# Performance work log

Hardware: AMD Instinct MI355X
Metric: run time of the kernel (lower is better)

The kernel has to match this reference:

```python
import jax, jax.numpy as jnp
import numpy as np

N, E, F, HID, HEADS, G = 20000, 320000, 64, 64, 4, 64
HC = HEADS * HID  # 256
NHID, NOUT = 256, 128
INV_SQRT2 = 0.7071067811865476


def _gat(x, src, dst, W, a_s, a_d, bias):
    # GATConv (v1), eval mode (no dropout); src/dst already include self-loops (PyG default)
    H, C = a_s.shape
    h = (x @ W).reshape(-1, H, C)  # [N,H,C]
    al_s = jnp.einsum('nhc,hc->nh', h, a_s)
    al_d = jnp.einsum('nhc,hc->nh', h, a_d)
    e = jax.nn.leaky_relu(al_s[src] + al_d[dst], 0.2)  # [Etot,H]
    m = jax.ops.segment_max(e, dst, num_segments=N)
    ex = jnp.exp(e - m[dst])
    den = jax.ops.segment_sum(ex, dst, num_segments=N)
    coef = ex / den[dst]  # softmax over incoming edges per target node
    out = jax.ops.segment_sum(h[src] * coef[:, :, None], dst, num_segments=N)
    return out.reshape(-1, H * C) + bias


def _bn(h, g, b):
    # BatchNorm1d, training-mode stats (biased var), eps=1e-5
    mu = h.mean(axis=0)
    var = h.var(axis=0)
    return g * (h - mu) * jax.lax.rsqrt(var + 1e-5) + b


def _block(x, src, dst, W1, a1s, a1d, b1, g1, be1, W2, a2s, a2d, b2, g2, be2, Wr, br, Wf, bf):
    h = jax.nn.relu(_bn(_gat(x, src, dst, W1, a1s, a1d, b1), g1, be1))
    h = jax.nn.relu(_bn(_gat(h, src, dst, W2, a2s, a2d, b2), g2, be2))
    res = x @ Wr + br
    return ((h + res) * INV_SQRT2) @ Wf + bf


def setup_inputs():
    ks = iter(jax.random.split(jax.random.key(0), 64))
    def rn(shape, scale=0.05):
        return jax.random.normal(next(ks), shape, dtype=jnp.float32) * scale
    inp = {}
    inp['x'] = jax.random.normal(next(ks), (N, F), dtype=jnp.float32)
    inp['edge_index'] = jax.random.randint(next(ks), (2, E), 0, N, dtype=jnp.int32)
    inp['batch'] = jnp.sort(jax.random.randint(next(ks), (N,), 0, G, dtype=jnp.int32))
    for b, cin in enumerate([F, HID]):
        p = 'b%d_' % b
        inp[p + 'W1'] = rn((cin, HC)); inp[p + 'a1s'] = rn((HEADS, HID)); inp[p + 'a1d'] = rn((HEADS, HID))
        inp[p + 'b1'] = jnp.zeros((HC,), jnp.float32)
        inp[p + 'g1'] = jnp.ones((HC,), jnp.float32); inp[p + 'be1'] = jnp.zeros((HC,), jnp.float32)
        inp[p + 'W2'] = rn((HC, HC)); inp[p + 'a2s'] = rn((1, HC)); inp[p + 'a2d'] = rn((1, HC))
        inp[p + 'b2'] = jnp.zeros((HC,), jnp.float32)
        inp[p + 'g2'] = jnp.ones((HC,), jnp.float32); inp[p + 'be2'] = jnp.zeros((HC,), jnp.float32)
        inp[p + 'Wr'] = rn((cin, HC)); inp[p + 'br'] = jnp.zeros((HC,), jnp.float32)
        inp[p + 'Wf'] = rn((HC, HID)); inp[p + 'bf'] = jnp.zeros((HID,), jnp.float32)
    inp['Wh1'] = rn((HID, NHID)); inp['bh1'] = jnp.zeros((NHID,), jnp.float32)
    inp['Wh2'] = rn((NHID, NOUT)); inp['bh2'] = jnp.zeros((NOUT,), jnp.float32)
    return inp


def reference(x, edge_index, batch,
              b0_W1, b0_a1s, b0_a1d, b0_b1, b0_g1, b0_be1, b0_W2, b0_a2s, b0_a2d, b0_b2, b0_g2, b0_be2, b0_Wr, b0_br, b0_Wf, b0_bf,
              b1_W1, b1_a1s, b1_a1d, b1_b1, b1_g1, b1_be1, b1_W2, b1_a2s, b1_a2d, b1_b2, b1_g2, b1_be2, b1_Wr, b1_br, b1_Wf, b1_bf,
              Wh1, bh1, Wh2, bh2):
    loops = jnp.arange(N, dtype=edge_index.dtype)
    src = jnp.concatenate([edge_index[0], loops])
    dst = jnp.concatenate([edge_index[1], loops])
    x = _block(x, src, dst, b0_W1, b0_a1s, b0_a1d, b0_b1, b0_g1, b0_be1, b0_W2, b0_a2s, b0_a2d, b0_b2, b0_g2, b0_be2, b0_Wr, b0_br, b0_Wf, b0_bf)
    x = _block(x, src, dst, b1_W1, b1_a1s, b1_a1d, b1_b1, b1_g1, b1_be1, b1_W2, b1_a2s, b1_a2d, b1_b2, b1_g2, b1_be2, b1_Wr, b1_br, b1_Wf, b1_bf)
    cnt = jax.ops.segment_sum(jnp.ones((N,), x.dtype), batch, num_segments=G)
    pooled = jax.ops.segment_sum(x, batch, num_segments=G) / jnp.maximum(cnt, 1.0)[:, None]
    h = jax.nn.relu(pooled @ Wh1 + bh1)
    return h @ Wh2 + bh2
```

## Files before the change

kernel.cpp:

```cpp
#include <hip/hip_runtime.h>

#define N_NODES 20000
#define N_EDGES 320000
#define ETOT (N_EDGES + N_NODES)
#define G_GROUPS 64

__device__ __forceinline__ unsigned short f2bf(float f) {
    unsigned int u = __float_as_uint(f);
    u += 0x7fffu + ((u >> 16) & 1u);
    return (unsigned short)(u >> 16);
}
__device__ __forceinline__ float bf2f(unsigned short v) {
    return __uint_as_float(((unsigned int)v) << 16);
}


__global__ __launch_bounds__(256) void k_hist(const int* __restrict__ ei, int* __restrict__ counts) {
    int e = blockIdx.x * 256 + threadIdx.x;
    if (e >= ETOT) return;
    int dst = (e < N_EDGES) ? ei[N_EDGES + e] : (e - N_EDGES);
    atomicAdd(&counts[dst], 1);
}

__global__ __launch_bounds__(1024) void k_scan(const int* __restrict__ counts, int* __restrict__ offs,
                                               int* __restrict__ cursor) {
    __shared__ int sdata[1024];
    const int t = threadIdx.x;
    const int chunk = (N_NODES + 1023) / 1024;
    int base = t * chunk;
    int s = 0;
    for (int i = 0; i < chunk; i++) { int idx = base + i; if (idx < N_NODES) s += counts[idx]; }
    sdata[t] = s;
    __syncthreads();
    for (int off = 1; off < 1024; off <<= 1) {
        int v = (t >= off) ? sdata[t - off] : 0;
        __syncthreads();
        sdata[t] += v;
        __syncthreads();
    }
    int prefix = (t == 0) ? 0 : sdata[t - 1];
    for (int i = 0; i < chunk; i++) {
        int idx = base + i;
        if (idx < N_NODES) {
            int cv = counts[idx];
            offs[idx] = prefix;
            cursor[idx] = prefix;
            prefix += cv;
        }
    }
    if (t == 1023) offs[N_NODES] = sdata[1023];
}

__global__ __launch_bounds__(256) void k_scatter(const int* __restrict__ ei, int* __restrict__ cursor,
                                                 int* __restrict__ csr_src) {
    int e = blockIdx.x * 256 + threadIdx.x;
    if (e >= ETOT) return;
    int src = (e < N_EDGES) ? ei[e] : (e - N_EDGES);
    int dst = (e < N_EDGES) ? ei[N_EDGES + e] : (e - N_EDGES);
    int p = atomicAdd(&cursor[dst], 1);
    csr_src[p] = src;
}


__global__ __launch_bounds__(256) void k_gemm64_dual(const float* __restrict__ x, const float* __restrict__ W1,
                                                     const float* __restrict__ Wr, const float* __restrict__ br,
                                                     const float* __restrict__ a_s, const float* __restrict__ a_d,
                                                     unsigned short* __restrict__ hbf, float* __restrict__ res,
                                                     float* __restrict__ alS, float* __restrict__ alD) {
    const int rb = blockIdx.x >> 2, cs = blockIdx.x & 3;
    const int row0 = rb * 64;
    const int nrows = min(64, N_NODES - row0);
    const int t = threadIdx.x;
    __shared__ float xs[32 * 68];
    __shared__ float b1s[32 * 64];
    __shared__ float brs[32 * 64];
    const int lane = t & 63;
    const int c0 = (t & 15) * 4;
    const int r0 = (t >> 4) * 4;
    const int rl = (t & 15) | ((t >> 6) << 4);
    const int c4 = (t >> 4) & 3;
    float acc1[4][4] = {}, acc2[4][4] = {};
    for (int k0 = 0; k0 < 64; k0 += 32) {
        if (k0) __syncthreads();
        {
            #pragma unroll
            for (int jj = 0; jj < 2; jj++) {
                int cc = c4 + 4 * jj;
                float4 v = {0.f, 0.f, 0.f, 0.f};
                if (rl < nrows) v = *(const float4*)(x + (row0 + rl) * 64 + k0 + cc * 4);
                xs[(cc * 4 + 0) * 68 + rl] = v.x;
                xs[(cc * 4 + 1) * 68 + rl] = v.y;
                xs[(cc * 4 + 2) * 68 + rl] = v.z;
                xs[(cc * 4 + 3) * 68 + rl] = v.w;
            }
        }
        {
            int cc = (t & 15) * 4;
            int k = t >> 4;
            #pragma unroll
            for (int pass = 0; pass < 2; pass++, k += 16) {
                *(float4*)(b1s + k * 64 + cc) = *(const float4*)(W1 + (k0 + k) * 256 + cs * 64 + cc);
                *(float4*)(brs + k * 64 + cc) = *(const float4*)(Wr + (k0 + k) * 256 + cs * 64 + cc);
            }
        }
        __syncthreads();
        #pragma unroll 8
        for (int k = 0; k < 32; k++) {
            float4 av = *(const float4*)(xs + k * 68 + r0);
            float4 b1 = *(const float4*)(b1s + k * 64 + c0);
            float4 b2 = *(const float4*)(brs + k * 64 + c0);
            float a[4] = {av.x, av.y, av.z, av.w};
            #pragma unroll
            for (int i = 0; i < 4; i++) {
                acc1[i][0] += a[i] * b1.x; acc1[i][1] += a[i] * b1.y;
                acc1[i][2] += a[i] * b1.z; acc1[i][3] += a[i] * b1.w;
                acc2[i][0] += a[i] * b2.x; acc2[i][1] += a[i] * b2.y;
                acc2[i][2] += a[i] * b2.z; acc2[i][3] += a[i] * b2.w;
            }
        }
    }
    const int gcol = cs * 64 + c0;
    float4 bv = *(const float4*)(br + gcol);
    float4 asv = *(const float4*)(a_s + gcol);
    float4 adv = *(const float4*)(a_d + gcol);
    #pragma unroll
    for (int i = 0; i < 4; i++) {
        int gr = row0 + r0 + i;
        bool ok = (r0 + i) < nrows;
        float4 o1 = {acc1[i][0], acc1[i][1], acc1[i][2], acc1[i][3]};
        if (ok) {
            ushort4 hq = {f2bf(o1.x), f2bf(o1.y), f2bf(o1.z), f2bf(o1.w)};
            *(ushort4*)(hbf + gr * 256 + gcol) = hq;
            float4 o2 = {acc2[i][0] + bv.x, acc2[i][1] + bv.y, acc2[i][2] + bv.z, acc2[i][3] + bv.w};
            *(float4*)(res + gr * 256 + gcol) = o2;
        }
        float ps = o1.x * asv.x + o1.y * asv.y + o1.z * asv.z + o1.w * asv.w;
        float pd = o1.x * adv.x + o1.y * adv.y + o1.z * adv.z + o1.w * adv.w;
        #pragma unroll
        for (int off = 8; off > 0; off >>= 1) {
            ps += __shfl_down(ps, off);
            pd += __shfl_down(pd, off);
        }
        if (((lane & 15) == 0) && ok) {
            alS[gr * 4 + cs] = ps;
            alD[gr * 4 + cs] = pd;
        }
    }
}


template <int H>
__global__ __launch_bounds__(256) void k_agg(const unsigned short* __restrict__ hbf, const float* __restrict__ alS,
                                             const float* __restrict__ alD, const int* __restrict__ offs,
                                             const int* __restrict__ csr_src, const float* __restrict__ bias,
                                             float* __restrict__ out) {
    int node = blockIdx.x * 4 + (threadIdx.x >> 6);
    int lane = threadIdx.x & 63;
    if (node >= N_NODES) return;
    const int head = (H == 4) ? (lane >> 4) : 0;
    const float ald = alD[node * H + head];
    int e0 = offs[node], e1 = offs[node + 1];
    const unsigned short* hp = hbf + lane * 4;
    float den = 0.f, a0 = 0.f, a1 = 0.f, a2 = 0.f, a3 = 0.f;
    int e = e0;
    for (; e + 8 <= e1; e += 8) {
        int s[8];
        #pragma unroll
        for (int i = 0; i < 8; i++) s[i] = csr_src[e + i];
        ushort4 hq[8];
        #pragma unroll
        for (int i = 0; i < 8; i++) hq[i] = *(const ushort4*)(hp + s[i] * 256);
        float w[8];
        #pragma unroll
        for (int i = 0; i < 8; i++) {
            float v = alS[s[i] * H + head] + ald;
            v = (v > 0.f) ? v : 0.2f * v;
            w[i] = __expf(v);
        }
        #pragma unroll
        for (int i = 0; i < 8; i++) {
            den += w[i];
            a0 += w[i] * bf2f(hq[i].x); a1 += w[i] * bf2f(hq[i].y);
            a2 += w[i] * bf2f(hq[i].z); a3 += w[i] * bf2f(hq[i].w);
        }
    }
    for (; e < e1; e++) {
        int s = csr_src[e];
        float v = alS[s * H + head] + ald;
        v = (v > 0.f) ? v : 0.2f * v;
        float w = __expf(v);
        ushort4 hq = *(const ushort4*)(hp + s * 256);
        den += w;
        a0 += w * bf2f(hq.x); a1 += w * bf2f(hq.y); a2 += w * bf2f(hq.z); a3 += w * bf2f(hq.w);
    }
    float inv = 1.f / den;
    const float4 bv = *(const float4*)(bias + lane * 4);
    float4 o = {a0 * inv + bv.x, a1 * inv + bv.y, a2 * inv + bv.z, a3 * inv + bv.w};
    *(float4*)(out + node * 256 + lane * 4) = o;
}


__global__ __launch_bounds__(256) void k_bnstats_fin(const float* __restrict__ x, float* __restrict__ sum,
                                                     float* __restrict__ sumsq, const float* __restrict__ g,
                                                     const float* __restrict__ be, float* __restrict__ scale,
                                                     float* __restrict__ shift, int* __restrict__ counter) {
    const int c = threadIdx.x;
    float s = 0.f, q = 0.f;
    for (int r = blockIdx.x; r < N_NODES; r += gridDim.x) {
        float v = x[r * 256 + c];
        s += v; q += v * v;
    }
    atomicAdd(&sum[c], s);
    atomicAdd(&sumsq[c], q);
    __threadfence();
    __syncthreads();
    __shared__ int lastFlag;
    if (c == 0) lastFlag = (atomicAdd(counter, 1) == (int)gridDim.x - 1);
    __syncthreads();
    if (lastFlag) {
        float S = atomicAdd(&sum[c], 0.f);
        float Q = atomicAdd(&sumsq[c], 0.f);
        float mu = S * (1.f / N_NODES);
        float var = Q * (1.f / N_NODES) - mu * mu;
        float sc = g[c] * rsqrtf(var + 1e-5f);
        scale[c] = sc;
        shift[c] = be[c] - mu * sc;
        sum[c] = 0.f;
        sumsq[c] = 0.f;
        if (c == 0) *counter = 0;
    }
}


__global__ __launch_bounds__(256) void k_gemm256(const float* __restrict__ A, const float* __restrict__ scale,
                                                 const float* __restrict__ shift, const float* __restrict__ B,
                                                 const float* __restrict__ a_s, const float* __restrict__ a_d,
                                                 unsigned short* __restrict__ C, float* __restrict__ alSp,
                                                 float* __restrict__ alDp) {
    const int rb = blockIdx.x >> 2, cs = blockIdx.x & 3;
    const int row0 = rb * 64;
    const int col0 = cs * 64;
    const int nrows = min(64, N_NODES - row0);
    const int t = threadIdx.x;
    __shared__ float xs[32 * 68];
    __shared__ float bs[32 * 64];
    __shared__ float scs[256], shs[256];
    scs[t] = scale[t];
    shs[t] = shift[t];
    const int lane = t & 63;
    const int rl = (t & 15) | ((t >> 6) << 4);
    const int c4 = (t >> 4) & 3;
    const int c0 = (t & 15) * 4;
    const int r0 = (t >> 4) * 4;
    float acc[4][4] = {};
    for (int k0 = 0; k0 < 256; k0 += 32) {
        __syncthreads();
        {
            #pragma unroll
            for (int jj = 0; jj < 2; jj++) {
                int cc = c4 + 4 * jj;
                int kcol = k0 + cc * 4;
                float4 w = {0.f, 0.f, 0.f, 0.f};
                if (rl < nrows) {
                    float4 v = *(const float4*)(A + (row0 + rl) * 256 + kcol);
                    w.x = fmaxf(v.x * scs[kcol + 0] + shs[kcol + 0], 0.f);
                    w.y = fmaxf(v.y * scs[kcol + 1] + shs[kcol + 1], 0.f);
                    w.z = fmaxf(v.z * scs[kcol + 2] + shs[kcol + 2], 0.f);
                    w.w = fmaxf(v.w * scs[kcol + 3] + shs[kcol + 3], 0.f);
                }
                xs[(cc * 4 + 0) * 68 + rl] = w.x;
                xs[(cc * 4 + 1) * 68 + rl] = w.y;
                xs[(cc * 4 + 2) * 68 + rl] = w.z;
                xs[(cc * 4 + 3) * 68 + rl] = w.w;
            }
        }
        {
            int ccB = (t & 15) * 4;
            int kB = t >> 4;
            #pragma unroll
            for (int pass = 0; pass < 2; pass++, kB += 16) {
                *(float4*)(bs + kB * 64 + ccB) = *(const float4*)(B + (k0 + kB) * 256 + col0 + ccB);
            }
        }
        __syncthreads();
        #pragma unroll 8
        for (int k = 0; k < 32; k++) {
            float4 av = *(const float4*)(xs + k * 68 + r0);
            float4 bv = *(const float4*)(bs + k * 64 + c0);
            float a[4] = {av.x, av.y, av.z, av.w};
            #pragma unroll
            for (int i = 0; i < 4; i++) {
                acc[i][0] += a[i] * bv.x; acc[i][1] += a[i] * bv.y;
                acc[i][2] += a[i] * bv.z; acc[i][3] += a[i] * bv.w;
            }
        }
    }
    float4 asv = *(const float4*)(a_s + col0 + c0);
    float4 adv = *(const float4*)(a_d + col0 + c0);
    #pragma unroll
    for (int i = 0; i < 4; i++) {
        int gr = row0 + r0 + i;
        bool ok = (r0 + i) < nrows;
        float4 o = {acc[i][0], acc[i][1], acc[i][2], acc[i][3]};
        if (ok) {
            ushort4 hq = {f2bf(o.x), f2bf(o.y), f2bf(o.z), f2bf(o.w)};
            *(ushort4*)(C + gr * 256 + col0 + c0) = hq;
        }
        float ps = o.x * asv.x + o.y * asv.y + o.z * asv.z + o.w * asv.w;
        float pd = o.x * adv.x + o.y * adv.y + o.z * adv.z + o.w * adv.w;
        #pragma unroll
        for (int off = 8; off > 0; off >>= 1) {
            ps += __shfl_down(ps, off);
            pd += __shfl_down(pd, off);
        }
        if (((lane & 15) == 0) && ok) {
            alSp[cs * N_NODES + gr] = ps;
            alDp[cs * N_NODES + gr] = pd;
        }
    }
}

__global__ __launch_bounds__(256) void k_alred(const float* __restrict__ alSp, const float* __restrict__ alDp,
                                               float* __restrict__ alS, float* __restrict__ alD) {
    int n = blockIdx.x * 256 + threadIdx.x;
    if (n >= N_NODES) return;
    alS[n] = (alSp[n] + alSp[N_NODES + n]) + (alSp[2 * N_NODES + n] + alSp[3 * N_NODES + n]);
    alD[n] = (alDp[n] + alDp[N_NODES + n]) + (alDp[2 * N_NODES + n] + alDp[3 * N_NODES + n]);
}


__global__ __launch_bounds__(256) void k_gemm_final(const float* __restrict__ A, const float* __restrict__ scale,
                                                    const float* __restrict__ shift, const float* __restrict__ res,
                                                    const float* __restrict__ B, const float* __restrict__ bias,
                                                    float* __restrict__ y) {
    const int row0 = blockIdx.x * 32;
    const int t = threadIdx.x;
    const float INVS = 0.70710678118654752440f;
    __shared__ float xs[32 * 36];
    __shared__ float bs[32 * 64];
    __shared__ float scs[256], shs[256];
    scs[t] = scale[t];
    shs[t] = shift[t];
    const int rf = (t & 15) | ((t >> 7) << 4);
    const int cf = (t >> 4) & 7;
    const int c0 = (t & 15) * 4;
    const int r0 = (t >> 4) * 2;
    float acc[2][4] = {};
    for (int k0 = 0; k0 < 256; k0 += 32) {
        __syncthreads();
        {
            int kcol = k0 + cf * 4;
            int gi = (row0 + rf) * 256 + kcol;
            float4 v = *(const float4*)(A + gi);
            float4 rv = *(const float4*)(res + gi);
            xs[(cf * 4 + 0) * 36 + rf] = (fmaxf(v.x * scs[kcol + 0] + shs[kcol + 0], 0.f) + rv.x) * INVS;
            xs[(cf * 4 + 1) * 36 + rf] = (fmaxf(v.y * scs[kcol + 1] + shs[kcol + 1], 0.f) + rv.y) * INVS;
            xs[(cf * 4 + 2) * 36 + rf] = (fmaxf(v.z * scs[kcol + 2] + shs[kcol + 2], 0.f) + rv.z) * INVS;
            xs[(cf * 4 + 3) * 36 + rf] = (fmaxf(v.w * scs[kcol + 3] + shs[kcol + 3], 0.f) + rv.w) * INVS;
        }
        {
            int cc = (t & 15) * 4;
            int k = t >> 4;
            #pragma unroll
            for (int pass = 0; pass < 2; pass++, k += 16) {
                *(float4*)(bs + k * 64 + cc) = *(const float4*)(B + (k0 + k) * 64 + cc);
            }
        }
        __syncthreads();
        #pragma unroll 8
        for (int k = 0; k < 32; k++) {
            float2 av = *(const float2*)(xs + k * 36 + r0);
            float4 bv = *(const float4*)(bs + k * 64 + c0);
            acc[0][0] += av.x * bv.x; acc[0][1] += av.x * bv.y;
            acc[0][2] += av.x * bv.z; acc[0][3] += av.x * bv.w;
            acc[1][0] += av.y * bv.x; acc[1][1] += av.y * bv.y;
            acc[1][2] += av.y * bv.z; acc[1][3] += av.y * bv.w;
        }
    }
    float4 bv = *(const float4*)(bias + c0);
    #pragma unroll
    for (int i = 0; i < 2; i++) {
        int gr = row0 + r0 + i;
        float4 o = {acc[i][0] + bv.x, acc[i][1] + bv.y, acc[i][2] + bv.z, acc[i][3] + bv.w};
        *(float4*)(y + gr * 64 + c0) = o;
    }
}


__global__ __launch_bounds__(256) void k_pool_head(const float* __restrict__ x, const int* __restrict__ batch,
                                                   const float* __restrict__ Wh1, const float* __restrict__ bh1,
                                                   const float* __restrict__ Wh2, const float* __restrict__ bh2,
                                                   float* __restrict__ out) {
    const int g = blockIdx.x;
    const int t = threadIdx.x;
    int lo = 0, hi = N_NODES;
    while (lo < hi) { int mid = (lo + hi) >> 1; if (batch[mid] < g) lo = mid + 1; else hi = mid; }
    int start = lo;
    hi = N_NODES;
    while (lo < hi) { int mid = (lo + hi) >> 1; if (batch[mid] < g + 1) lo = mid + 1; else hi = mid; }
    int end = lo;
    float cnt = (float)(end - start);

    __shared__ float part[256];
    __shared__ float p[64];
    __shared__ float hrow[256];
    const int c = t & 63;
    float s = 0.f;
    for (int r = start + (t >> 6); r < end; r += 4) s += x[r * 64 + c];
    part[t] = s;
    __syncthreads();
    if (t < 64) {
        float v = part[t] + part[t + 64] + part[t + 128] + part[t + 192];
        p[t] = v / fmaxf(cnt, 1.f);
    }
    __syncthreads();
    float a = bh1[t];
    #pragma unroll 8
    for (int k = 0; k < 64; k++) a += p[k] * Wh1[k * 256 + t];
    hrow[t] = fmaxf(a, 0.f);
    __syncthreads();
    if (t < 128) {
        float o = bh2[t];
        #pragma unroll 8
        for (int k = 0; k < 256; k++) o += hrow[k] * Wh2[k * 128 + t];
        out[g * 128 + t] = o;
    }
}


extern "C" void kernel_launch(void* const* d_in, const int* in_sizes, int n_in,
                              void* d_out, int out_size, void* d_ws, size_t ws_size,
                              hipStream_t stream) {
    (void)in_sizes; (void)n_in; (void)out_size; (void)ws_size;
    const float* x0 = (const float*)d_in[0];
    const int* ei = (const int*)d_in[1];
    const int* batch = (const int*)d_in[2];
    const float* Wh1 = (const float*)d_in[35];
    const float* bh1 = (const float*)d_in[36];
    const float* Wh2 = (const float*)d_in[37];
    const float* bh2 = (const float*)d_in[38];

    char* p = (char*)d_ws;
    auto alloc = [&](size_t bytes) -> void* {
        void* r = (void*)p;
        p += (bytes + 255) & ~(size_t)255;
        return r;
    };
    int* counts = (int*)alloc((size_t)N_NODES * 4);
    float* bnsum = (float*)alloc(2048);
    float* bnsq = bnsum + 256;
    int* bncnt = (int*)alloc(256);
    const size_t zero_bytes = (((size_t)N_NODES * 4 + 255) & ~(size_t)255) + 2048 + 256;
    int* offs = (int*)alloc((size_t)(N_NODES + 1) * 4);
    int* cursor = (int*)alloc((size_t)N_NODES * 4);
    int* csr_src = (int*)alloc((size_t)ETOT * 4);
    float* alS = (float*)alloc((size_t)N_NODES * 4 * 4);
    float* alD = (float*)alloc((size_t)N_NODES * 4 * 4);
    float* alSp = (float*)alloc((size_t)N_NODES * 4 * 4);
    float* alDp = (float*)alloc((size_t)N_NODES * 4 * 4);
    float* scaleb = (float*)alloc(1024);
    float* shiftb = (float*)alloc(1024);
    unsigned short* hbuf = (unsigned short*)alloc((size_t)N_NODES * 256 * 2);
    float* obuf = (float*)alloc((size_t)N_NODES * 256 * 4);
    float* rbuf = (float*)alloc((size_t)N_NODES * 256 * 4);
    float* xout = (float*)alloc((size_t)N_NODES * 64 * 4);

    hipMemsetAsync(counts, 0, zero_bytes, stream);
    k_hist<<<(ETOT + 255) / 256, 256, 0, stream>>>(ei, counts);
    k_scan<<<1, 1024, 0, stream>>>(counts, offs, cursor);
    k_scatter<<<(ETOT + 255) / 256, 256, 0, stream>>>(ei, cursor, csr_src);

    const int tile64_blocks = ((N_NODES + 63) / 64) * 4;
    const int node_blocks = (N_NODES + 3) / 4;
    const int red_blocks = (N_NODES + 255) / 256;
    const int final_blocks = N_NODES / 32;

    auto run_block = [&](const float* xin, int base) {
        const float* W1 = (const float*)d_in[base + 0];
        const float* a1s = (const float*)d_in[base + 1];
        const float* a1d = (const float*)d_in[base + 2];
        const float* b1 = (const float*)d_in[base + 3];
        const float* g1 = (const float*)d_in[base + 4];
        const float* be1 = (const float*)d_in[base + 5];
        const float* W2 = (const float*)d_in[base + 6];
        const float* a2s = (const float*)d_in[base + 7];
        const float* a2d = (const float*)d_in[base + 8];
        const float* b2 = (const float*)d_in[base + 9];
        const float* g2 = (const float*)d_in[base + 10];
        const float* be2 = (const float*)d_in[base + 11];
        const float* Wr = (const float*)d_in[base + 12];
        const float* br = (const float*)d_in[base + 13];
        const float* Wf = (const float*)d_in[base + 14];
        const float* bf = (const float*)d_in[base + 15];

        k_gemm64_dual<<<tile64_blocks, 256, 0, stream>>>(xin, W1, Wr, br, a1s, a1d, hbuf, rbuf, alS, alD);
        k_agg<4><<<node_blocks, 256, 0, stream>>>(hbuf, alS, alD, offs, csr_src, b1, obuf);
        k_bnstats_fin<<<256, 256, 0, stream>>>(obuf, bnsum, bnsq, g1, be1, scaleb, shiftb, bncnt);
        k_gemm256<<<tile64_blocks, 256, 0, stream>>>(obuf, scaleb, shiftb, W2, a2s, a2d, hbuf, alSp, alDp);
        k_alred<<<red_blocks, 256, 0, stream>>>(alSp, alDp, alS, alD);
        k_agg<1><<<node_blocks, 256, 0, stream>>>(hbuf, alS, alD, offs, csr_src, b2, obuf);
        k_bnstats_fin<<<256, 256, 0, stream>>>(obuf, bnsum, bnsq, g2, be2, scaleb, shiftb, bncnt);
        k_gemm_final<<<final_blocks, 256, 0, stream>>>(obuf, scaleb, shiftb, rbuf, Wf, bf, xout);
    };

    run_block(x0, 3);
    run_block(xout, 19);

    k_pool_head<<<G_GROUPS, 256, 0, stream>>>(xout, batch, Wh1, bh1, Wh2, bh2, (float*)d_out);
}
```

Before: 675.1 us.

## Use bf16 MFMA for the 256x256 GAT GEMM with prepacked weight fragments

Replaces the fp32 scalar-FMA 256-wide GEMM with a bf16 MFMA 16x16x32 kernel. The weight matrix is converted once per call into MFMA fragment order and held in registers. The activation tile is BN-ReLU transformed, packed to bf16 and staged in shared memory. Attention partial dot products now come out per 16-column tile, which needs 16 partials per node and a wider reduction in k_alred. This trades fp32 precision on the GEMM inputs for matrix-core throughput, and adds two small prep kernels.

```diff
diff --git a/kernel.cpp b/kernel.cpp
--- a/kernel.cpp
+++ b/kernel.cpp
@@ -5,6 +5,9 @@
 #define ETOT (N_EDGES + N_NODES)
 #define G_GROUPS 64
 
+typedef __attribute__((ext_vector_type(8))) short bf16x8;
+typedef __attribute__((ext_vector_type(4))) float f32x4;
+
 __device__ __forceinline__ unsigned short f2bf(float f) {
     unsigned int u = __float_as_uint(f);
     u += 0x7fffu + ((u >> 16) & 1u);
@@ -12,6 +15,9 @@
 }
 __device__ __forceinline__ float bf2f(unsigned short v) {
     return __uint_as_float(((unsigned int)v) << 16);
+}
+__device__ __forceinline__ unsigned int pack2bf(float a, float b) {
+    return (unsigned int)f2bf(a) | ((unsigned int)f2bf(b) << 16);
 }
 
 
@@ -232,90 +238,109 @@
 }
 
 
-__global__ __launch_bounds__(256) void k_gemm256(const float* __restrict__ A, const float* __restrict__ scale,
-                                                 const float* __restrict__ shift, const float* __restrict__ B,
-                                                 const float* __restrict__ a_s, const float* __restrict__ a_d,
-                                                 unsigned short* __restrict__ C, float* __restrict__ alSp,
-                                                 float* __restrict__ alDp) {
+__global__ __launch_bounds__(256) void k_prepB(const float* __restrict__ W, unsigned short* __restrict__ Bf) {
+    int s = blockIdx.x * 256 + threadIdx.x;
+    int l = s & 63;
+    int nt = (s >> 6) & 15;
+    int kt = s >> 10;
+    int n = nt * 16 + (l & 15);
+    int kb = kt * 32 + (l >> 4) * 8;
+    float v[8];
+    #pragma unroll
+    for (int j = 0; j < 8; j++) v[j] = W[(kb + j) * 256 + n];
+    uint4 q = {pack2bf(v[0], v[1]), pack2bf(v[2], v[3]), pack2bf(v[4], v[5]), pack2bf(v[6], v[7])};
+    *(uint4*)(Bf + s * 8) = q;
+}
+
+
+__global__ __launch_bounds__(256) void k_gemm256_mfma(const float* __restrict__ A, const float* __restrict__ scale,
+                                                      const float* __restrict__ shift,
+                                                      const unsigned short* __restrict__ Bf,
+                                                      const float* __restrict__ a_s, const float* __restrict__ a_d,
+                                                      unsigned short* __restrict__ C, float* __restrict__ alSp,
+                                                      float* __restrict__ alDp) {
     const int rb = blockIdx.x >> 2, cs = blockIdx.x & 3;
     const int row0 = rb * 64;
-    const int col0 = cs * 64;
     const int nrows = min(64, N_NODES - row0);
     const int t = threadIdx.x;
-    __shared__ float xs[32 * 68];
-    __shared__ float bs[32 * 64];
+    const int w = t >> 6;
+    const int l = t & 63;
+    const int quad = l >> 4;
+    const int colLocal = l & 15;
+    __shared__ unsigned short As[2 * 4 * 64 * 8];
     __shared__ float scs[256], shs[256];
     scs[t] = scale[t];
     shs[t] = shift[t];
-    const int lane = t & 63;
-    const int rl = (t & 15) | ((t >> 6) << 4);
-    const int c4 = (t >> 4) & 3;
-    const int c0 = (t & 15) * 4;
-    const int r0 = (t >> 4) * 4;
-    float acc[4][4] = {};
-    for (int k0 = 0; k0 < 256; k0 += 32) {
-        __syncthreads();
-        {
+
+    const int ntg = cs * 4 + w;
+    bf16x8 bfrag[8];
+    #pragma unroll
+    for (int kt = 0; kt < 8; kt++)
+        bfrag[kt] = *(const bf16x8*)(Bf + ((kt * 16 + ntg) * 64 + l) * 8);
+
+    f32x4 acc[4];
+    #pragma unroll
+    for (int mt = 0; mt < 4; mt++) acc[mt] = (f32x4){0.f, 0.f, 0.f, 0.f};
+
+    const int smt = (t >> 6) & 3;
+    const int sm = smt * 16 + (l & 15);
+    const int skoff = (l >> 4) * 8;
+
+    for (int kc = 0; kc < 4; kc++) {
+        __syncthreads();
+        #pragma unroll
+        for (int kt2 = 0; kt2 < 2; kt2++) {
+            int k = kc * 64 + kt2 * 32 + skoff;
+            float4 v0 = {0.f, 0.f, 0.f, 0.f}, v1 = {0.f, 0.f, 0.f, 0.f};
+            if (sm < nrows) {
+                v0 = *(const float4*)(A + (row0 + sm) * 256 + k);
+                v1 = *(const float4*)(A + (row0 + sm) * 256 + k + 4);
+                v0.x = fmaxf(v0.x * scs[k + 0] + shs[k + 0], 0.f);
+                v0.y = fmaxf(v0.y * scs[k + 1] + shs[k + 1], 0.f);
+                v0.z = fmaxf(v0.z * scs[k + 2] + shs[k + 2], 0.f);
+                v0.w = fmaxf(v0.w * scs[k + 3] + shs[k + 3], 0.f);
+                v1.x = fmaxf(v1.x * scs[k + 4] + shs[k + 4], 0.f);
+                v1.y = fmaxf(v1.y * scs[k + 5] + shs[k + 5], 0.f);
+                v1.z = fmaxf(v1.z * scs[k + 6] + shs[k + 6], 0.f);
+                v1.w = fmaxf(v1.w * scs[k + 7] + shs[k + 7], 0.f);
+            }
+            uint4 q = {pack2bf(v0.x, v0.y), pack2bf(v0.z, v0.w), pack2bf(v1.x, v1.y), pack2bf(v1.z, v1.w)};
+            *(uint4*)(As + ((kt2 * 4 + smt) * 64 + l) * 8) = q;
+        }
+        __syncthreads();
+        #pragma unroll
+        for (int kt2 = 0; kt2 < 2; kt2++) {
+            int ktg = kc * 2 + kt2;
             #pragma unroll
-            for (int jj = 0; jj < 2; jj++) {
-                int cc = c4 + 4 * jj;
-                int kcol = k0 + cc * 4;
-                float4 w = {0.f, 0.f, 0.f, 0.f};
-                if (rl < nrows) {
-                    float4 v = *(const float4*)(A + (row0 + rl) * 256 + kcol);
-                    w.x = fmaxf(v.x * scs[kcol + 0] + shs[kcol + 0], 0.f);
-                    w.y = fmaxf(v.y * scs[kcol + 1] + shs[kcol + 1], 0.f);
-                    w.z = fmaxf(v.z * scs[kcol + 2] + shs[kcol + 2], 0.f);
-                    w.w = fmaxf(v.w * scs[kcol + 3] + shs[kcol + 3], 0.f);
-                }
-                xs[(cc * 4 + 0) * 68 + rl] = w.x;
-                xs[(cc * 4 + 1) * 68 + rl] = w.y;
-                xs[(cc * 4 + 2) * 68 + rl] = w.z;
-                xs[(cc * 4 + 3) * 68 + rl] = w.w;
-            }
-        }
-        {
-            int ccB = (t & 15) * 4;
-            int kB = t >> 4;
+            for (int mt = 0; mt < 4; mt++) {
+                bf16x8 af = *(const bf16x8*)(As + ((kt2 * 4 + mt) * 64 + l) * 8);
+                acc[mt] = __builtin_amdgcn_mfma_f32_16x16x32_bf16(af, bfrag[ktg], acc[mt], 0, 0, 0);
+            }
+        }
+    }
+
+    const int col = cs * 64 + w * 16 + colLocal;
+    const float asv = a_s[col];
+    const float adv = a_d[col];
+    #pragma unroll
+    for (int mt = 0; mt < 4; mt++) {
+        #pragma unroll
+        for (int r = 0; r < 4; r++) {
+            float v = acc[mt][r];
+            int lr = mt * 16 + quad * 4 + r;
+            bool ok = lr < nrows;
+            int row = row0 + lr;
+            if (ok) C[row * 256 + col] = f2bf(v);
+            float ps = v * asv, pd = v * adv;
             #pragma unroll
-            for (int pass = 0; pass < 2; pass++, kB += 16) {
-                *(float4*)(bs + kB * 64 + ccB) = *(const float4*)(B + (k0 + kB) * 256 + col0 + ccB);
-            }
-        }
-        __syncthreads();
-        #pragma unroll 8
-        for (int k = 0; k < 32; k++) {
-            float4 av = *(const float4*)(xs + k * 68 + r0);
-            float4 bv = *(const float4*)(bs + k * 64 + c0);
-            float a[4] = {av.x, av.y, av.z, av.w};
-            #pragma unroll
-            for (int i = 0; i < 4; i++) {
-                acc[i][0] += a[i] * bv.x; acc[i][1] += a[i] * bv.y;
-                acc[i][2] += a[i] * bv.z; acc[i][3] += a[i] * bv.w;
-            }
-        }
-    }
-    float4 asv = *(const float4*)(a_s + col0 + c0);
-    float4 adv = *(const float4*)(a_d + col0 + c0);
-    #pragma unroll
-    for (int i = 0; i < 4; i++) {
-        int gr = row0 + r0 + i;
-        bool ok = (r0 + i) < nrows;
-        float4 o = {acc[i][0], acc[i][1], acc[i][2], acc[i][3]};
-        if (ok) {
-            ushort4 hq = {f2bf(o.x), f2bf(o.y), f2bf(o.z), f2bf(o.w)};
-            *(ushort4*)(C + gr * 256 + col0 + c0) = hq;
-        }
-        float ps = o.x * asv.x + o.y * asv.y + o.z * asv.z + o.w * asv.w;
-        float pd = o.x * adv.x + o.y * adv.y + o.z * adv.z + o.w * adv.w;
-        #pragma unroll
-        for (int off = 8; off > 0; off >>= 1) {
-            ps += __shfl_down(ps, off);
-            pd += __shfl_down(pd, off);
-        }
-        if (((lane & 15) == 0) && ok) {
-            alSp[cs * N_NODES + gr] = ps;
-            alDp[cs * N_NODES + gr] = pd;
+            for (int off = 1; off < 16; off <<= 1) {
+                ps += __shfl_xor(ps, off);
+                pd += __shfl_xor(pd, off);
+            }
+            if (colLocal == 0 && ok) {
+                alSp[ntg * N_NODES + row] = ps;
+                alDp[ntg * N_NODES + row] = pd;
+            }
         }
     }
 }
@@ -324,8 +349,14 @@
                                                float* __restrict__ alS, float* __restrict__ alD) {
     int n = blockIdx.x * 256 + threadIdx.x;
     if (n >= N_NODES) return;
-    alS[n] = (alSp[n] + alSp[N_NODES + n]) + (alSp[2 * N_NODES + n] + alSp[3 * N_NODES + n]);
-    alD[n] = (alDp[n] + alDp[N_NODES + n]) + (alDp[2 * N_NODES + n] + alDp[3 * N_NODES + n]);
+    float s = 0.f, d = 0.f;
+    #pragma unroll
+    for (int i = 0; i < 16; i++) {
+        s += alSp[i * N_NODES + n];
+        d += alDp[i * N_NODES + n];
+    }
+    alS[n] = s;
+    alD[n] = d;
 }
 
 
@@ -456,33 +487,36 @@
     int* csr_src = (int*)alloc((size_t)ETOT * 4);
     float* alS = (float*)alloc((size_t)N_NODES * 4 * 4);
     float* alD = (float*)alloc((size_t)N_NODES * 4 * 4);
-    float* alSp = (float*)alloc((size_t)N_NODES * 4 * 4);
-    float* alDp = (float*)alloc((size_t)N_NODES * 4 * 4);
+    float* alSp = (float*)alloc((size_t)N_NODES * 16 * 4);
+    float* alDp = (float*)alloc((size_t)N_NODES * 16 * 4);
     float* scaleb = (float*)alloc(1024);
     float* shiftb = (float*)alloc(1024);
     unsigned short* hbuf = (unsigned short*)alloc((size_t)N_NODES * 256 * 2);
     float* obuf = (float*)alloc((size_t)N_NODES * 256 * 4);
     float* rbuf = (float*)alloc((size_t)N_NODES * 256 * 4);
     float* xout = (float*)alloc((size_t)N_NODES * 64 * 4);
+    unsigned short* Bf0 = (unsigned short*)alloc(256 * 256 * 2);
+    unsigned short* Bf1 = (unsigned short*)alloc(256 * 256 * 2);
 
     hipMemsetAsync(counts, 0, zero_bytes, stream);
     k_hist<<<(ETOT + 255) / 256, 256, 0, stream>>>(ei, counts);
     k_scan<<<1, 1024, 0, stream>>>(counts, offs, cursor);
     k_scatter<<<(ETOT + 255) / 256, 256, 0, stream>>>(ei, cursor, csr_src);
+    k_prepB<<<32, 256, 0, stream>>>((const float*)d_in[3 + 6], Bf0);
+    k_prepB<<<32, 256, 0, stream>>>((const float*)d_in[19 + 6], Bf1);
 
     const int tile64_blocks = ((N_NODES + 63) / 64) * 4;
     const int node_blocks = (N_NODES + 3) / 4;
     const int red_blocks = (N_NODES + 255) / 256;
     const int final_blocks = N_NODES / 32;
 
-    auto run_block = [&](const float* xin, int base) {
+    auto run_block = [&](const float* xin, int base, const unsigned short* Bf) {
         const float* W1 = (const float*)d_in[base + 0];
         const float* a1s = (const float*)d_in[base + 1];
         const float* a1d = (const float*)d_in[base + 2];
         const float* b1 = (const float*)d_in[base + 3];
         const float* g1 = (const float*)d_in[base + 4];
         const float* be1 = (const float*)d_in[base + 5];
-        const float* W2 = (const float*)d_in[base + 6];
         const float* a2s = (const float*)d_in[base + 7];
         const float* a2d = (const float*)d_in[base + 8];
         const float* b2 = (const float*)d_in[base + 9];
@@ -496,15 +530,15 @@
         k_gemm64_dual<<<tile64_blocks, 256, 0, stream>>>(xin, W1, Wr, br, a1s, a1d, hbuf, rbuf, alS, alD);
         k_agg<4><<<node_blocks, 256, 0, stream>>>(hbuf, alS, alD, offs, csr_src, b1, obuf);
         k_bnstats_fin<<<256, 256, 0, stream>>>(obuf, bnsum, bnsq, g1, be1, scaleb, shiftb, bncnt);
-        k_gemm256<<<tile64_blocks, 256, 0, stream>>>(obuf, scaleb, shiftb, W2, a2s, a2d, hbuf, alSp, alDp);
+        k_gemm256_mfma<<<tile64_blocks, 256, 0, stream>>>(obuf, scaleb, shiftb, Bf, a2s, a2d, hbuf, alSp, alDp);
         k_alred<<<red_blocks, 256, 0, stream>>>(alSp, alDp, alS, alD);
         k_agg<1><<<node_blocks, 256, 0, stream>>>(hbuf, alS, alD, offs, csr_src, b2, obuf);
         k_bnstats_fin<<<256, 256, 0, stream>>>(obuf, bnsum, bnsq, g2, be2, scaleb, shiftb, bncnt);
         k_gemm_final<<<final_blocks, 256, 0, stream>>>(obuf, scaleb, shiftb, rbuf, Wf, bf, xout);
     };
 
-    run_block(x0, 3);
-    run_block(xout, 19);
+    run_block(x0, 3, Bf0);
+    run_block(xout, 19, Bf1);
 
     k_pool_head<<<G_GROUPS, 256, 0, stream>>>(xout, batch, Wh1, bh1, Wh2, bh2, (float*)d_out);
 }
```

Result: faster. 635.1 us (-5.9%).
